# Kernel optimization log

Measured on AMD Instinct MI355X. Metric: run time of the kernel, lower is better.

Reference implementation:

```python
import jax, jax.numpy as jnp
import numpy as np

B, NS, NF, T, D = 64, 2, 13, 24, 512
H = 8
DH = D // H
DFF = 2048
EPS = 1e-5


def setup_inputs() -> dict:
    key = jax.random.key(0)
    ks = jax.random.split(key, 16)
    s = 0.02
    inp = {
        'x': jax.random.normal(ks[0], (B, NS * NF, T, D), jnp.float32),
        'w_in_s': jax.random.normal(ks[1], (3 * D, D), jnp.float32) * s,
        'b_in_s': jnp.zeros((3 * D,), jnp.float32),
        'w_out_s': jax.random.normal(ks[2], (D, D), jnp.float32) * s,
        'b_out_s': jnp.zeros((D,), jnp.float32),
        'w_in_f': jax.random.normal(ks[3], (3 * D, D), jnp.float32) * s,
        'b_in_f': jnp.zeros((3 * D,), jnp.float32),
        'w_out_f': jax.random.normal(ks[4], (D, D), jnp.float32) * s,
        'b_out_f': jnp.zeros((D,), jnp.float32),
        'w1': jax.random.normal(ks[5], (DFF, D), jnp.float32) * s,
        'b1': jnp.zeros((DFF,), jnp.float32),
        'w2': jax.random.normal(ks[6], (D, DFF), jnp.float32) * s,
        'b2': jnp.zeros((D,), jnp.float32),
        'g1': jnp.ones((D,), jnp.float32), 'be1': jnp.zeros((D,), jnp.float32),
        'g2': jnp.ones((D,), jnp.float32), 'be2': jnp.zeros((D,), jnp.float32),
        'g3': jnp.ones((D,), jnp.float32), 'be3': jnp.zeros((D,), jnp.float32),
    }
    return inp


def _layer_norm(x, g, b):
    mu = jnp.mean(x, axis=-1, keepdims=True)
    var = jnp.mean(jnp.square(x - mu), axis=-1, keepdims=True)
    return (x - mu) * jax.lax.rsqrt(var + EPS) * g + b


def _mha(x, w_in, b_in, w_out, b_out):
    # x: [..., S, D]; torch nn.MultiheadAttention math, eval mode (no dropout)
    qkv = x @ w_in.T + b_in                     # [..., S, 3D]
    q, k, v = jnp.split(qkv, 3, axis=-1)
    shp = q.shape[:-1] + (H, DH)
    q, k, v = q.reshape(shp), k.reshape(shp), v.reshape(shp)
    scores = jnp.einsum('...qhd,...khd->...hqk', q, k) / np.sqrt(DH).astype(np.float32)
    a = jax.nn.softmax(scores, axis=-1)
    o = jnp.einsum('...hqk,...khd->...qhd', a, v).reshape(x.shape)
    return o @ w_out.T + b_out


def reference(x, w_in_s, b_in_s, w_out_s, b_out_s, w_in_f, b_in_f, w_out_f, b_out_f,
              w1, b1, w2, b2, g1, be1, g2, be2, g3, be3):
    xr = x.reshape(B, NS, NF, T, D)
    # station attention: attend over the NS axis for each (feature, t)
    xs = xr.transpose(0, 2, 3, 1, 4)            # [B, NF, T, NS, D]
    xs = xs + _mha(xs, w_in_s, b_in_s, w_out_s, b_out_s)
    x = xs.transpose(0, 3, 1, 2, 4).reshape(B, NS * NF, T, D)
    x = _layer_norm(x, g1, be1)
    # feature attention: attend over the NF axis for each (station, t)
    xr = x.reshape(B, NS, NF, T, D)
    xf = xr.transpose(0, 1, 3, 2, 4)            # [B, NS, T, NF, D]
    xf = xf + _mha(xf, w_in_f, b_in_f, w_out_f, b_out_f)
    x = xf.transpose(0, 1, 3, 2, 4).reshape(B, NS * NF, T, D)
    x = _layer_norm(x, g2, be2)
    # feed-forward
    ff = jax.nn.relu(x @ w1.T + b1) @ w2.T + b2
    x = _layer_norm(x + ff, g3, be3)
    return x
```

## Files before the change

### kernel.cpp

```cpp
#include <hip/hip_runtime.h>
#include <stdint.h>

typedef unsigned short u16;
typedef __bf16 bf16x8 __attribute__((ext_vector_type(8)));
typedef float f32x4 __attribute__((ext_vector_type(4)));

#define DEV __device__ __forceinline__

DEV float bf2f(u16 u) {
    union { uint32_t u; float f; } c; c.u = ((uint32_t)u) << 16; return c.f;
}
DEV u16 f2bf(float f) {
    union { float f; uint32_t u; } c; c.f = f;
    uint32_t u = c.u;
    u += 0x7FFFu + ((u >> 16) & 1u);
    return (u16)(u >> 16);
}

DEV void gload_lds16(const u16* gp, u16* lp) {
    __builtin_amdgcn_global_load_lds(
        (__attribute__((address_space(1))) u16*)(uintptr_t)gp,
        (__attribute__((address_space(3))) u16*)lp,
        16, 0, 0);
}

#define WAITVM4 asm volatile("s_waitcnt vmcnt(4)" ::: "memory")
#define WAITVM0 asm volatile("s_waitcnt vmcnt(0)" ::: "memory")
#define MEMFENCE asm volatile("" ::: "memory")

DEV void load16f(const u16* p, float* f) {
    uint4 a = *reinterpret_cast<const uint4*>(p);
    uint4 b = *reinterpret_cast<const uint4*>(p + 8);
    uint32_t w[8] = { a.x, a.y, a.z, a.w, b.x, b.y, b.z, b.w };
#pragma unroll
    for (int k = 0; k < 8; ++k) {
        union { uint32_t u; float f; } lo, hi;
        lo.u = w[k] << 16; hi.u = w[k] & 0xFFFF0000u;
        f[2 * k] = lo.f; f[2 * k + 1] = hi.f;
    }
}
DEV float dot16(const u16* p, const float* q) {
    uint4 a = *reinterpret_cast<const uint4*>(p);
    uint4 b = *reinterpret_cast<const uint4*>(p + 8);
    uint32_t w[8] = { a.x, a.y, a.z, a.w, b.x, b.y, b.z, b.w };
    float d = 0.0f;
#pragma unroll
    for (int k = 0; k < 8; ++k) {
        union { uint32_t u; float f; } lo, hi;
        lo.u = w[k] << 16; hi.u = w[k] & 0xFFFF0000u;
        d += q[2 * k] * lo.f;
        d += q[2 * k + 1] * hi.f;
    }
    return d;
}
DEV void fma16(const u16* p, float pw, float* acc) {
    uint4 a = *reinterpret_cast<const uint4*>(p);
    uint4 b = *reinterpret_cast<const uint4*>(p + 8);
    uint32_t w[8] = { a.x, a.y, a.z, a.w, b.x, b.y, b.z, b.w };
#pragma unroll
    for (int k = 0; k < 8; ++k) {
        union { uint32_t u; float f; } lo, hi;
        lo.u = w[k] << 16; hi.u = w[k] & 0xFFFF0000u;
        acc[2 * k] += pw * lo.f;
        acc[2 * k + 1] += pw * hi.f;
    }
}
DEV void store16(u16* p, const float* y) {
    uint32_t w[8];
#pragma unroll
    for (int k = 0; k < 8; ++k)
        w[k] = (uint32_t)f2bf(y[2 * k]) | ((uint32_t)f2bf(y[2 * k + 1]) << 16);
    uint4 a = { w[0], w[1], w[2], w[3] };
    uint4 b = { w[4], w[5], w[6], w[7] };
    *reinterpret_cast<uint4*>(p) = a;
    *reinterpret_cast<uint4*>(p + 8) = b;
}

__global__ __launch_bounds__(256) void k_f32_to_bf16(
    const float* __restrict__ in, u16* __restrict__ out, int n4)
{
    int i = blockIdx.x * 256 + threadIdx.x;
    if (i >= n4) return;
    float4 v = reinterpret_cast<const float4*>(in)[i];
    ushort4 o;
    o.x = f2bf(v.x); o.y = f2bf(v.y); o.z = f2bf(v.z); o.w = f2bf(v.w);
    reinterpret_cast<ushort4*>(out)[i] = o;
}

template<bool RELU, bool RESID, int NT>
__global__ __launch_bounds__(512, 2) void k_gemm8p(
    const u16* __restrict__ A, const u16* __restrict__ W,
    const float* __restrict__ bias, const u16* __restrict__ res,
    u16* __restrict__ C, int M, int N, int K)
{
    __shared__ __align__(16) u16 Abuf[2][16384];
    __shared__ __align__(16) u16 Bbuf[2][16384];

    const int tid  = threadIdx.x;
    const int lane = tid & 63;
    const int wave = tid >> 6;
    const int wm   = wave >> 2;
    const int wn   = wave & 3;
    const int l15  = lane & 15;
    const int lg   = lane >> 4;

    const int nwg = gridDim.x;
    const int v = (blockIdx.x & 7) * (nwg >> 3) + (blockIdx.x >> 3);
    const long tileM = (long)(v / NT) * 256;
    const long tileN = (long)(v % NT) * 256;

    const int nIter = K >> 7;

    f32x4 acc[8][4] = {};

    const long Abase = (tileM + (tid >> 3)) * (long)K + (((tid & 7) ^ ((tid >> 3) & 7)) << 3);
    const long Bbase = (tileN + (tid >> 3)) * (long)K + (((tid & 7) ^ ((tid >> 3) & 7)) << 3);

    auto stA = [&](int h, int t) {
#pragma unroll
        for (int e = 0; e < 2; ++e)
            gload_lds16(A + Abase + (long)(h * 128 + e * 64) * K + t * 64,
                        &Abuf[t & 1][(h * 1024 + e * 512 + tid) * 8]);
    };
    auto stB = [&](int h, int t) {
#pragma unroll
        for (int e = 0; e < 2; ++e)
            gload_lds16(W + Bbase + (long)(h * 128 + e * 64) * K + t * 64,
                        &Bbuf[t & 1][(h * 1024 + e * 512 + tid) * 8]);
    };

    int koff[2];
#pragma unroll
    for (int ks = 0; ks < 2; ++ks)
        koff[ks] = ((ks * 4 + lg) ^ (l15 & 7)) * 8;
    const int aRow = wm * 128 + l15;
    const int bRow = wn * 64 + l15;

    stA(0, 0); stA(1, 0); stB(0, 0); stB(1, 0); stB(0, 1); stB(1, 1);
    WAITVM4;
    MEMFENCE;
    __builtin_amdgcn_s_barrier();
    MEMFENCE;

    bf16x8 b[4][2];

    for (int j = 0; j < nIter; ++j) {
        const bool pre = (j + 1 < nIter);
        const int E = 2 * j;
#pragma unroll
        for (int ph = 0; ph < 8; ++ph) {
            const int bb = ph >> 2;
            const int q  = ph & 3;
            if (q == 0) {
#pragma unroll
                for (int n = 0; n < 4; ++n)
#pragma unroll
                    for (int ks = 0; ks < 2; ++ks)
                        b[n][ks] = *reinterpret_cast<const bf16x8*>(
                            &Bbuf[bb][(bRow + n * 16) * 64 + koff[ks]]);
            }
            bf16x8 aq[2][2];
#pragma unroll
            for (int mi = 0; mi < 2; ++mi)
#pragma unroll
                for (int ks = 0; ks < 2; ++ks)
                    aq[mi][ks] = *reinterpret_cast<const bf16x8*>(
                        &Abuf[bb][(aRow + (q * 2 + mi) * 16) * 64 + koff[ks]]);
            if (ph == 0) stA(0, E + 1);
            else if (ph == 1) stA(1, E + 1);
            else if (ph == 2) { if (pre) stB(0, E + 2); }
            else if (ph == 3) {
                if (pre) { stB(1, E + 2); WAITVM4; } else { WAITVM0; }
            }
            else if (ph == 4) { if (pre) stA(0, E + 2); }
            else if (ph == 5) { if (pre) stA(1, E + 2); }
            else if (ph == 6) { if (pre) stB(0, E + 3); }
            else {
                if (pre) { stB(1, E + 3); WAITVM4; } else { WAITVM0; }
            }
            MEMFENCE;
            __builtin_amdgcn_s_barrier();
            MEMFENCE;
            __builtin_amdgcn_s_setprio(1);
#pragma unroll
            for (int mi = 0; mi < 2; ++mi)
#pragma unroll
                for (int n = 0; n < 4; ++n)
#pragma unroll
                    for (int ks = 0; ks < 2; ++ks)
                        acc[q * 2 + mi][n] = __builtin_amdgcn_mfma_f32_16x16x32_bf16(
                            aq[mi][ks], b[n][ks], acc[q * 2 + mi][n], 0, 0, 0);
            __builtin_amdgcn_s_setprio(0);
            MEMFENCE;
            __builtin_amdgcn_s_barrier();
            MEMFENCE;
        }
    }

    const int crow0 = (int)tileM + wm * 128 + ((lane >> 4) << 2);
    const int ccol0 = (int)tileN + wn * 64 + l15;
#pragma unroll
    for (int m = 0; m < 8; ++m) {
#pragma unroll
        for (int n = 0; n < 4; ++n) {
            const int col = ccol0 + n * 16;
            const float bv = bias[col];
#pragma unroll
            for (int r = 0; r < 4; ++r) {
                const long row = crow0 + m * 16 + r;
                float vv = acc[m][n][r] + bv;
                if (RESID) vv += bf2f(res[row * N + col]);
                if (RELU)  vv = fmaxf(vv, 0.0f);
                C[row * N + col] = f2bf(vv);
            }
        }
    }
}

template<bool RELU, bool RESID, int NT>
__global__ __launch_bounds__(256) void k_gemm(
    const u16* __restrict__ A, const u16* __restrict__ W,
    const float* __restrict__ bias, const u16* __restrict__ res,
    u16* __restrict__ C, int M, int N, int K)
{
    __shared__ __align__(16) u16 As[2 * 128 * 32];
    __shared__ __align__(16) u16 Bs[2 * 128 * 32];

    const int tid  = threadIdx.x;
    const int lane = tid & 63;
    const int wave = tid >> 6;
    const int wm   = wave >> 1;
    const int wn   = wave & 1;

    const int bid = blockIdx.x;
    const int xcd = bid & 7;
    const int j0  = bid >> 3;
    const long tileM = (long)(xcd * 39 + j0 / NT) * 128;
    const long tileN = (long)(j0 % NT) * 128;

    f32x4 acc[4][4] = {};

    const int r4 = tid >> 2;
    const int c8 = ((tid & 3) ^ ((tid >> 3) & 3)) * 8;
    const u16* Ab = A + (tileM + r4) * (long)K + c8;
    const u16* Wb = W + (tileN + r4) * (long)K + c8;
    const int dst0 = wave * 512;

    const int arow = wm * 64 + (lane & 15);
    const int brow = wn * 64 + (lane & 15);
    const int koff = ((lane >> 4) ^ ((lane >> 1) & 3)) * 8;

    auto stage = [&](int buf, int kk) {
        u16* a0 = As + buf * 4096 + dst0;
        u16* b0 = Bs + buf * 4096 + dst0;
        gload_lds16(Ab + kk,                a0);
        gload_lds16(Ab + kk + (long)64 * K, a0 + 2048);
        gload_lds16(Wb + kk,                b0);
        gload_lds16(Wb + kk + (long)64 * K, b0 + 2048);
    };
    auto compute = [&](int buf) {
        const u16* ab = As + buf * 4096;
        const u16* bb = Bs + buf * 4096;
        bf16x8 a[4], b[4];
#pragma unroll
        for (int f = 0; f < 4; ++f) {
            a[f] = *reinterpret_cast<const bf16x8*>(&ab[(arow + f * 16) * 32 + koff]);
            b[f] = *reinterpret_cast<const bf16x8*>(&bb[(brow + f * 16) * 32 + koff]);
        }
#pragma unroll
        for (int i = 0; i < 4; ++i)
#pragma unroll
            for (int j = 0; j < 4; ++j)
                acc[i][j] = __builtin_amdgcn_mfma_f32_16x16x32_bf16(
                    a[i], b[j], acc[i][j], 0, 0, 0);
    };

    stage(0, 0);
    __syncthreads();

    int cur = 0;
    for (int kk = 0; kk < K - 32; kk += 32) {
        stage(cur ^ 1, kk + 32);
        compute(cur);
        __syncthreads();
        cur ^= 1;
    }
    compute(cur);

    const int crow = (int)tileM + wm * 64 + ((lane >> 4) << 2);
    const int ccol = (int)tileN + wn * 64 + (lane & 15);
#pragma unroll
    for (int i = 0; i < 4; ++i) {
#pragma unroll
        for (int j = 0; j < 4; ++j) {
            const int col = ccol + j * 16;
            const float bv = bias[col];
#pragma unroll
            for (int r = 0; r < 4; ++r) {
                const long row = crow + i * 16 + r;
                float v = acc[i][j][r] + bv;
                if (RESID) v += bf2f(res[row * N + col]);
                if (RELU)  v = fmaxf(v, 0.0f);
                C[row * N + col] = f2bf(v);
            }
        }
    }
}

__global__ __launch_bounds__(256) void k_attn_s(
    const u16* __restrict__ qkv, u16* __restrict__ o)
{
    const int wave = threadIdx.x >> 6, lane = threadIdx.x & 63;
    const int g = blockIdx.x * 4 + wave;
    const int t = g % 24, bf = g / 24, f = bf % 13, b = bf / 13;
    const int base = b * 624 + f * 24 + t;
    const int h = lane >> 3, i = (lane >> 2) & 1, c = lane & 3;
    const int off = h * 64 + c * 16;

    float qf[16];
    load16f(qkv + (size_t)(base + i * 312) * 1536 + off, qf);

    float s[2];
#pragma unroll
    for (int j = 0; j < 2; ++j) {
        float d = dot16(qkv + (size_t)(base + j * 312) * 1536 + 512 + off, qf);
        d += __shfl_xor(d, 1);
        d += __shfl_xor(d, 2);
        s[j] = d * 0.125f;
    }
    const float m = fmaxf(s[0], s[1]);
    const float e0 = expf(s[0] - m), e1 = expf(s[1] - m);
    const float inv = 1.0f / (e0 + e1);
    const float p0 = e0 * inv, p1 = e1 * inv;

    float acc[16] = {};
    fma16(qkv + (size_t)base * 1536 + 1024 + off, p0, acc);
    fma16(qkv + (size_t)(base + 312) * 1536 + 1024 + off, p1, acc);

    store16(o + (size_t)(base + i * 312) * 512 + off, acc);
}

__global__ __launch_bounds__(256) void k_attn_f(
    const u16* __restrict__ qkv, u16* __restrict__ o)
{
    const int wave = threadIdx.x >> 6, lane = threadIdx.x & 63;
    const int p = blockIdx.x * 4 + wave;
    const int h = p & 7, g = p >> 3;
    const int t = g % 24, bs = g / 24, st = bs % 2, b = bs / 2;
    const int base = b * 624 + st * 312 + t;
    const int i = lane >> 2, c = lane & 3;
    const int iq = (i < 13) ? i : 12;
    const int off = h * 64 + c * 16;

    float qf[16];
    load16f(qkv + (size_t)(base + iq * 24) * 1536 + off, qf);

    float sc[13];
#pragma unroll
    for (int j = 0; j < 13; ++j) {
        float d = dot16(qkv + (size_t)(base + j * 24) * 1536 + 512 + off, qf);
        d += __shfl_xor(d, 1);
        d += __shfl_xor(d, 2);
        sc[j] = d * 0.125f;
    }
    float m = sc[0];
#pragma unroll
    for (int j = 1; j < 13; ++j) m = fmaxf(m, sc[j]);
    float den = 0.0f;
#pragma unroll
    for (int j = 0; j < 13; ++j) { sc[j] = expf(sc[j] - m); den += sc[j]; }
    const float inv = 1.0f / den;

    float acc[16] = {};
#pragma unroll
    for (int j = 0; j < 13; ++j)
        fma16(qkv + (size_t)(base + j * 24) * 1536 + 1024 + off, sc[j], acc);
#pragma unroll
    for (int e = 0; e < 16; ++e) acc[e] *= inv;

    if (i < 13)
        store16(o + (size_t)(base + i * 24) * 512 + off, acc);
}

template<bool OUTF32>
__global__ __launch_bounds__(256) void k_ln(
    const u16* __restrict__ in, const float* __restrict__ g,
    const float* __restrict__ be, u16* __restrict__ outb,
    float* __restrict__ outf)
{
    const int row  = blockIdx.x * 4 + (threadIdx.x >> 6);
    const int lane = threadIdx.x & 63;
    const u16* p = in + (size_t)row * 512 + lane * 8;

    uint4 va = *reinterpret_cast<const uint4*>(p);
    uint32_t ua[4] = { va.x, va.y, va.z, va.w };
    float x[8];
#pragma unroll
    for (int i = 0; i < 4; ++i) {
        x[2 * i]     = bf2f((u16)(ua[i] & 0xFFFFu));
        x[2 * i + 1] = bf2f((u16)(ua[i] >> 16));
    }
    float s = 0.f, sq = 0.f;
#pragma unroll
    for (int i = 0; i < 8; ++i) { s += x[i]; sq += x[i] * x[i]; }
#pragma unroll
    for (int off = 32; off; off >>= 1) {
        s  += __shfl_xor(s, off);
        sq += __shfl_xor(sq, off);
    }
    const float mean = s * (1.0f / 512.0f);
    const float var  = sq * (1.0f / 512.0f) - mean * mean;
    const float rstd = rsqrtf(var + 1e-5f);

    const int col = lane * 8;
    float4 g0 = *reinterpret_cast<const float4*>(g + col);
    float4 g1 = *reinterpret_cast<const float4*>(g + col + 4);
    float4 b0 = *reinterpret_cast<const float4*>(be + col);
    float4 b1 = *reinterpret_cast<const float4*>(be + col + 4);
    float gg[8] = { g0.x, g0.y, g0.z, g0.w, g1.x, g1.y, g1.z, g1.w };
    float bb[8] = { b0.x, b0.y, b0.z, b0.w, b1.x, b1.y, b1.z, b1.w };

    float y[8];
#pragma unroll
    for (int i = 0; i < 8; ++i) y[i] = (x[i] - mean) * rstd * gg[i] + bb[i];

    if (OUTF32) {
        float4 o0 = { y[0], y[1], y[2], y[3] };
        float4 o1 = { y[4], y[5], y[6], y[7] };
        reinterpret_cast<float4*>(outf + (size_t)row * 512 + col)[0] = o0;
        reinterpret_cast<float4*>(outf + (size_t)row * 512 + col + 4)[0] = o1;
    } else {
        uint32_t w[4];
#pragma unroll
        for (int i = 0; i < 4; ++i)
            w[i] = (uint32_t)f2bf(y[2 * i]) | ((uint32_t)f2bf(y[2 * i + 1]) << 16);
        uint4 ov = { w[0], w[1], w[2], w[3] };
        *reinterpret_cast<uint4*>(outb + (size_t)row * 512 + col) = ov;
    }
}

extern "C" void kernel_launch(void* const* d_in, const int* in_sizes, int n_in,
                              void* d_out, int out_size, void* d_ws, size_t ws_size,
                              hipStream_t stream)
{
    const float* x       = (const float*)d_in[0];
    const float* w_in_s  = (const float*)d_in[1];
    const float* b_in_s  = (const float*)d_in[2];
    const float* w_out_s = (const float*)d_in[3];
    const float* b_out_s = (const float*)d_in[4];
    const float* w_in_f  = (const float*)d_in[5];
    const float* b_in_f  = (const float*)d_in[6];
    const float* w_out_f = (const float*)d_in[7];
    const float* b_out_f = (const float*)d_in[8];
    const float* w1      = (const float*)d_in[9];
    const float* b1      = (const float*)d_in[10];
    const float* w2      = (const float*)d_in[11];
    const float* b2      = (const float*)d_in[12];
    const float* g1      = (const float*)d_in[13];
    const float* be1     = (const float*)d_in[14];
    const float* g2      = (const float*)d_in[15];
    const float* be2     = (const float*)d_in[16];
    const float* g3      = (const float*)d_in[17];
    const float* be3     = (const float*)d_in[18];

    const int R = 39936;
    u16* xb   = (u16*)d_ws;
    u16* buf1 = xb + (size_t)R * 512;
    u16* obuf = buf1 + (size_t)R * 1536;
    u16* wqs  = buf1 + (size_t)R * 2048;
    u16* wos  = wqs + 1536 * 512;
    u16* wqf  = wos + 512 * 512;
    u16* wof  = wqf + 1536 * 512;
    u16* w1b  = wof + 512 * 512;
    u16* w2b  = w1b + 2048 * 512;

    auto conv = [&](const float* src, u16* dst, int n) {
        int n4 = n / 4;
        k_f32_to_bf16<<<dim3((n4 + 255) / 256), dim3(256), 0, stream>>>(src, dst, n4);
    };
    conv(x,       xb,  R * 512);
    conv(w_in_s,  wqs, 1536 * 512);
    conv(w_out_s, wos, 512 * 512);
    conv(w_in_f,  wqf, 1536 * 512);
    conv(w_out_f, wof, 512 * 512);
    conv(w1,      w1b, 2048 * 512);
    conv(w2,      w2b, 512 * 2048);

    const dim3 blk256(256);
    const dim3 blk512(512);

    k_gemm8p<false, false, 6><<<dim3(936), blk512, 0, stream>>>(
        xb, wqs, b_in_s, nullptr, buf1, R, 1536, 512);
    k_attn_s<<<dim3(19968 / 4), blk256, 0, stream>>>(buf1, obuf);
    k_gemm<false, true, 4><<<dim3(312 * 4), blk256, 0, stream>>>(
        obuf, wos, b_out_s, xb, xb, R, 512, 512);
    k_ln<false><<<dim3(R / 4), blk256, 0, stream>>>(xb, g1, be1, xb, nullptr);

    k_gemm8p<false, false, 6><<<dim3(936), blk512, 0, stream>>>(
        xb, wqf, b_in_f, nullptr, buf1, R, 1536, 512);
    k_attn_f<<<dim3(24576 / 4), blk256, 0, stream>>>(buf1, obuf);
    k_gemm<false, true, 4><<<dim3(312 * 4), blk256, 0, stream>>>(
        obuf, wof, b_out_f, xb, xb, R, 512, 512);
    k_ln<false><<<dim3(R / 4), blk256, 0, stream>>>(xb, g2, be2, xb, nullptr);

    k_gemm8p<true, false, 8><<<dim3(1248), blk512, 0, stream>>>(
        xb, w1b, b1, nullptr, buf1, R, 2048, 512);
    k_gemm8p<false, true, 2><<<dim3(312), blk512, 0, stream>>>(
        buf1, w2b, b2, xb, xb, R, 512, 2048);
    k_ln<true><<<dim3(R / 4), blk256, 0, stream>>>(xb, g3, be3, nullptr, (float*)d_out);
}
```

Baseline: 630.5 us.

## Replace out-projection GEMM with triple-buffered 256x128 tile kernel and use it for FFN2

Replaces the double-buffered 128x128, K=32 GEMM with a 512-thread kernel that uses 256x128 tiles, K=64 steps and three LDS stages filled by direct global-to-LDS loads. Loads are split into two phases per step, with explicit vmcnt waits, barriers and s_setprio around the MFMA blocks, to overlap memory with compute. The new kernel replaces both attention out-projection GEMMs and also the FFN second GEMM, which previously ran on the k_gemm8p kernel. The cost is larger LDS use, about 144KB per block, which limits occupancy.

```diff
diff --git a/kernel.cpp b/kernel.cpp
--- a/kernel.cpp
+++ b/kernel.cpp
@@ -24,6 +24,7 @@
         16, 0, 0);
 }
 
+#define WAITVM6 asm volatile("s_waitcnt vmcnt(6)" ::: "memory")
 #define WAITVM4 asm volatile("s_waitcnt vmcnt(4)" ::: "memory")
 #define WAITVM0 asm volatile("s_waitcnt vmcnt(0)" ::: "memory")
 #define MEMFENCE asm volatile("" ::: "memory")
@@ -218,90 +219,146 @@
 }
 
 template<bool RELU, bool RESID, int NT>
-__global__ __launch_bounds__(256) void k_gemm(
+__global__ __launch_bounds__(512, 2) void k_gemm3s(
     const u16* __restrict__ A, const u16* __restrict__ W,
     const float* __restrict__ bias, const u16* __restrict__ res,
     u16* __restrict__ C, int M, int N, int K)
 {
-    __shared__ __align__(16) u16 As[2 * 128 * 32];
-    __shared__ __align__(16) u16 Bs[2 * 128 * 32];
+    __shared__ __align__(16) u16 Abuf[3][16384];
+    __shared__ __align__(16) u16 Bbuf[3][8192];
 
     const int tid  = threadIdx.x;
     const int lane = tid & 63;
     const int wave = tid >> 6;
     const int wm   = wave >> 1;
     const int wn   = wave & 1;
-
-    const int bid = blockIdx.x;
-    const int xcd = bid & 7;
-    const int j0  = bid >> 3;
-    const long tileM = (long)(xcd * 39 + j0 / NT) * 128;
-    const long tileN = (long)(j0 % NT) * 128;
+    const int l15  = lane & 15;
+    const int lg   = lane >> 4;
+
+    const int nwg = gridDim.x;
+    const int v = (blockIdx.x & 7) * (nwg >> 3) + (blockIdx.x >> 3);
+    const long tileM = (long)(v / NT) * 256;
+    const long tileN = (long)(v % NT) * 128;
+
+    const int nT = K >> 6;
 
     f32x4 acc[4][4] = {};
 
-    const int r4 = tid >> 2;
-    const int c8 = ((tid & 3) ^ ((tid >> 3) & 3)) * 8;
-    const u16* Ab = A + (tileM + r4) * (long)K + c8;
-    const u16* Wb = W + (tileN + r4) * (long)K + c8;
-    const int dst0 = wave * 512;
-
-    const int arow = wm * 64 + (lane & 15);
-    const int brow = wn * 64 + (lane & 15);
-    const int koff = ((lane >> 4) ^ ((lane >> 1) & 3)) * 8;
-
-    auto stage = [&](int buf, int kk) {
-        u16* a0 = As + buf * 4096 + dst0;
-        u16* b0 = Bs + buf * 4096 + dst0;
-        gload_lds16(Ab + kk,                a0);
-        gload_lds16(Ab + kk + (long)64 * K, a0 + 2048);
-        gload_lds16(Wb + kk,                b0);
-        gload_lds16(Wb + kk + (long)64 * K, b0 + 2048);
+    const long Abase = (tileM + (tid >> 3)) * (long)K + (((tid & 7) ^ ((tid >> 3) & 7)) << 3);
+    const long Bbase = (tileN + (tid >> 3)) * (long)K + (((tid & 7) ^ ((tid >> 3) & 7)) << 3);
+
+    auto stage = [&](int t, int p) {
+        const int s = t % 3;
+        const long ko = (long)t * 64;
+        if (p == 0) {
+#pragma unroll
+            for (int e = 0; e < 3; ++e)
+                gload_lds16(A + Abase + (long)(e * 64) * K + ko,
+                            &Abuf[s][(e * 512 + tid) * 8]);
+        } else {
+            gload_lds16(A + Abase + (long)192 * K + ko,
+                        &Abuf[s][(3 * 512 + tid) * 8]);
+#pragma unroll
+            for (int e = 0; e < 2; ++e)
+                gload_lds16(W + Bbase + (long)(e * 64) * K + ko,
+                            &Bbuf[s][(e * 512 + tid) * 8]);
+        }
     };
-    auto compute = [&](int buf) {
-        const u16* ab = As + buf * 4096;
-        const u16* bb = Bs + buf * 4096;
-        bf16x8 a[4], b[4];
-#pragma unroll
-        for (int f = 0; f < 4; ++f) {
-            a[f] = *reinterpret_cast<const bf16x8*>(&ab[(arow + f * 16) * 32 + koff]);
-            b[f] = *reinterpret_cast<const bf16x8*>(&bb[(brow + f * 16) * 32 + koff]);
-        }
-#pragma unroll
-        for (int i = 0; i < 4; ++i)
-#pragma unroll
-            for (int j = 0; j < 4; ++j)
-                acc[i][j] = __builtin_amdgcn_mfma_f32_16x16x32_bf16(
-                    a[i], b[j], acc[i][j], 0, 0, 0);
-    };
-
-    stage(0, 0);
-    __syncthreads();
-
-    int cur = 0;
-    for (int kk = 0; kk < K - 32; kk += 32) {
-        stage(cur ^ 1, kk + 32);
-        compute(cur);
-        __syncthreads();
-        cur ^= 1;
-    }
-    compute(cur);
-
-    const int crow = (int)tileM + wm * 64 + ((lane >> 4) << 2);
-    const int ccol = (int)tileN + wn * 64 + (lane & 15);
-#pragma unroll
-    for (int i = 0; i < 4; ++i) {
-#pragma unroll
-        for (int j = 0; j < 4; ++j) {
-            const int col = ccol + j * 16;
+
+    int koff[2];
+#pragma unroll
+    for (int ks = 0; ks < 2; ++ks)
+        koff[ks] = ((ks * 4 + lg) ^ (l15 & 7)) * 8;
+    const int aRow = wm * 64 + l15;
+    const int bRow = wn * 64 + l15;
+
+    stage(0, 0); stage(0, 1);
+    stage(1, 0); stage(1, 1);
+    WAITVM6;
+    MEMFENCE;
+    __builtin_amdgcn_s_barrier();
+    MEMFENCE;
+
+    for (int j = 0; j < nT; ++j) {
+        const int s = j % 3;
+        const u16* ab = Abuf[s];
+        const u16* bb = Bbuf[s];
+        const bool pre = (j + 2 < nT);
+
+        bf16x8 bfr[4][2];
+#pragma unroll
+        for (int n = 0; n < 4; ++n)
+#pragma unroll
+            for (int ks = 0; ks < 2; ++ks)
+                bfr[n][ks] = *reinterpret_cast<const bf16x8*>(
+                    &bb[(bRow + n * 16) * 64 + koff[ks]]);
+        bf16x8 a0[2][2];
+#pragma unroll
+        for (int mi = 0; mi < 2; ++mi)
+#pragma unroll
+            for (int ks = 0; ks < 2; ++ks)
+                a0[mi][ks] = *reinterpret_cast<const bf16x8*>(
+                    &ab[(aRow + mi * 16) * 64 + koff[ks]]);
+        if (pre) stage(j + 2, 0);
+        MEMFENCE;
+        __builtin_amdgcn_s_barrier();
+        MEMFENCE;
+        __builtin_amdgcn_s_setprio(1);
+#pragma unroll
+        for (int mi = 0; mi < 2; ++mi)
+#pragma unroll
+            for (int n = 0; n < 4; ++n)
+#pragma unroll
+                for (int ks = 0; ks < 2; ++ks)
+                    acc[mi][n] = __builtin_amdgcn_mfma_f32_16x16x32_bf16(
+                        a0[mi][ks], bfr[n][ks], acc[mi][n], 0, 0, 0);
+        __builtin_amdgcn_s_setprio(0);
+        MEMFENCE;
+        __builtin_amdgcn_s_barrier();
+        MEMFENCE;
+
+        bf16x8 a1[2][2];
+#pragma unroll
+        for (int mi = 0; mi < 2; ++mi)
+#pragma unroll
+            for (int ks = 0; ks < 2; ++ks)
+                a1[mi][ks] = *reinterpret_cast<const bf16x8*>(
+                    &ab[(aRow + (2 + mi) * 16) * 64 + koff[ks]]);
+        if (pre) { stage(j + 2, 1); WAITVM6; }
+        else if (j + 1 < nT) { WAITVM0; }
+        MEMFENCE;
+        __builtin_amdgcn_s_barrier();
+        MEMFENCE;
+        __builtin_amdgcn_s_setprio(1);
+#pragma unroll
+        for (int mi = 0; mi < 2; ++mi)
+#pragma unroll
+            for (int n = 0; n < 4; ++n)
+#pragma unroll
+                for (int ks = 0; ks < 2; ++ks)
+                    acc[2 + mi][n] = __builtin_amdgcn_mfma_f32_16x16x32_bf16(
+                        a1[mi][ks], bfr[n][ks], acc[2 + mi][n], 0, 0, 0);
+        __builtin_amdgcn_s_setprio(0);
+        MEMFENCE;
+        __builtin_amdgcn_s_barrier();
+        MEMFENCE;
+    }
+
+    const int crow0 = (int)tileM + wm * 64 + ((lane >> 4) << 2);
+    const int ccol0 = (int)tileN + wn * 64 + l15;
+#pragma unroll
+    for (int m = 0; m < 4; ++m) {
+#pragma unroll
+        for (int n = 0; n < 4; ++n) {
+            const int col = ccol0 + n * 16;
             const float bv = bias[col];
 #pragma unroll
             for (int r = 0; r < 4; ++r) {
-                const long row = crow + i * 16 + r;
-                float v = acc[i][j][r] + bv;
-                if (RESID) v += bf2f(res[row * N + col]);
-                if (RELU)  v = fmaxf(v, 0.0f);
-                C[row * N + col] = f2bf(v);
+                const long row = crow0 + m * 16 + r;
+                float vv = acc[m][n][r] + bv;
+                if (RESID) vv += bf2f(res[row * N + col]);
+                if (RELU)  vv = fmaxf(vv, 0.0f);
+                C[row * N + col] = f2bf(vv);
             }
         }
     }
@@ -492,20 +549,20 @@
     k_gemm8p<false, false, 6><<<dim3(936), blk512, 0, stream>>>(
         xb, wqs, b_in_s, nullptr, buf1, R, 1536, 512);
     k_attn_s<<<dim3(19968 / 4), blk256, 0, stream>>>(buf1, obuf);
-    k_gemm<false, true, 4><<<dim3(312 * 4), blk256, 0, stream>>>(
+    k_gemm3s<false, true, 4><<<dim3(624), blk512, 0, stream>>>(
         obuf, wos, b_out_s, xb, xb, R, 512, 512);
     k_ln<false><<<dim3(R / 4), blk256, 0, stream>>>(xb, g1, be1, xb, nullptr);
 
     k_gemm8p<false, false, 6><<<dim3(936), blk512, 0, stream>>>(
         xb, wqf, b_in_f, nullptr, buf1, R, 1536, 512);
     k_attn_f<<<dim3(24576 / 4), blk256, 0, stream>>>(buf1, obuf);
-    k_gemm<false, true, 4><<<dim3(312 * 4), blk256, 0, stream>>>(
+    k_gemm3s<false, true, 4><<<dim3(624), blk512, 0, stream>>>(
         obuf, wof, b_out_f, xb, xb, R, 512, 512);
     k_ln<false><<<dim3(R / 4), blk256, 0, stream>>>(xb, g2, be2, xb, nullptr);
 
     k_gemm8p<true, false, 8><<<dim3(1248), blk512, 0, stream>>>(
         xb, w1b, b1, nullptr, buf1, R, 2048, 512);
-    k_gemm8p<false, true, 2><<<dim3(312), blk512, 0, stream>>>(
+    k_gemm3s<false, true, 4><<<dim3(624), blk512, 0, stream>>>(
         buf1, w2b, b2, xb, xb, R, 512, 2048);
     k_ln<true><<<dim3(R / 4), blk256, 0, stream>>>(xb, g3, be3, nullptr, (float*)d_out);
 }
```

After: 623.9 us. About the same (-1.0%).
